# Performance work log

Hardware: AMD Instinct MI355X
Metric: run time of the kernel (lower is better)

The kernel has to match this reference:

```python
import jax, jax.numpy as jnp
import numpy as np

N_NODES = 100000
N_EDGES = 1600000
D = 128
LAYERS = 3
LN_EPS = 1e-5


def setup_inputs() -> dict:
    key = jax.random.key(0)
    k1, k2, k3 = jax.random.split(key, 3)
    x = jax.random.normal(k1, (N_NODES, D), dtype=jnp.float32)
    edge_index = jax.random.randint(k2, (2, N_EDGES), 0, N_NODES, dtype=jnp.int64)
    W = jax.random.normal(k3, (LAYERS, D, D), dtype=jnp.float32) * (1.0 / np.sqrt(D))
    b = jnp.zeros((LAYERS, D), dtype=jnp.float32)
    ln_w = jnp.ones((LAYERS, D), dtype=jnp.float32)
    ln_b = jnp.zeros((LAYERS, D), dtype=jnp.float32)
    return {"x": x, "edge_index": edge_index, "W": W, "b": b, "ln_w": ln_w, "ln_b": ln_b}


def _gcn_conv(x, row, col, deg_inv_sqrt, W, b):
    # x: [N, D]; row/col: [E+N] (self-loops appended); PyG GCNConv math:
    # h = (D^-1/2 (A+I) D^-1/2) (x @ W) + b
    xw = x @ W  # [N, D]
    norm = deg_inv_sqrt[row] * deg_inv_sqrt[col]  # [E+N]
    msg = xw[row] * norm[:, None]  # gather + scale, memory-bound
    out = jax.ops.segment_sum(msg, col, num_segments=x.shape[0])  # scatter-add at targets
    return out + b


def _layer_norm(h, w, bset):
    mu = jnp.mean(h, axis=-1, keepdims=True)
    var = jnp.mean(jnp.square(h - mu), axis=-1, keepdims=True)
    return (h - mu) * jax.lax.rsqrt(var + LN_EPS) * w + bset


def reference(x, edge_index, W, b, ln_w, ln_b):
    n = x.shape[0]
    loops = jnp.arange(n, dtype=edge_index.dtype)
    row = jnp.concatenate([edge_index[0], loops])  # sources
    col = jnpp = jnp.concatenate([edge_index[1], loops])  # targets
    deg = jax.ops.segment_sum(jnp.ones_like(col, dtype=x.dtype), col, num_segments=n)
    deg_inv_sqrt = jax.lax.rsqrt(deg)  # deg >= 1 due to self-loops
    for i in range(LAYERS):
        h = _gcn_conv(x, row, col, deg_inv_sqrt, W[i], b[i])
        h = jax.nn.relu(h)
        h = h + x  # residual (shapes always match: in == emb)
        # dropout is identity in eval mode
        x = _layer_norm(h, ln_w[i], ln_b[i])
    return x
```

## Files before the change

kernel.cpp:

```cpp
#include <hip/hip_runtime.h>
#include <stdint.h>

#define NN 100000
#define NE 1600000
#define DD 128
#define NLAYERS 3
#define NB 196
#define BRS 9
#define NBLK 256
#define EPB 6250
#define CAP 96
#define ENTCAP 9216
#define OVFCAP 4096
#define AGG_BLOCKS 2048

typedef __attribute__((ext_vector_type(8))) short bf16x8;
typedef __attribute__((ext_vector_type(4))) float f32x4;
typedef __attribute__((ext_vector_type(4))) unsigned int u32x4;
typedef __attribute__((ext_vector_type(2))) unsigned int u32x2;

__device__ __forceinline__ float bflo(uint32_t v){ return __uint_as_float(v << 16); }
__device__ __forceinline__ float bfhi(uint32_t v){ return __uint_as_float(v & 0xFFFF0000u); }
__device__ __forceinline__ float bf1(unsigned short u){ return __uint_as_float(((uint32_t)u) << 16); }
__device__ __forceinline__ unsigned short f2bf(float f){
  uint32_t u = __float_as_uint(f);
  u += 0x7FFFu + ((u >> 16) & 1u);
  return (unsigned short)(u >> 16);
}
__device__ __forceinline__ int colof(int j){ return ((j & 7) << 4) | (j >> 3); }

__global__ __launch_bounds__(256) void k_detect(const uint32_t* __restrict__ x,
                                                const uint32_t* __restrict__ ei,
                                                int* __restrict__ flags,
                                                int* __restrict__ ovf_cnt,
                                                unsigned int* __restrict__ gmax){
  __shared__ int s_f32, s_i32;
  if (threadIdx.x == 0){
    s_f32 = 0; s_i32 = 0; *ovf_cnt = 0;
    gmax[0] = 0u; gmax[1] = 0u; gmax[2] = 0u;
  }
  __syncthreads();
  int f = 0, i32 = 0;
  for (int idx = threadIdx.x; idx < 8192; idx += 256){
    uint32_t u = x[idx];
    if (((u >> 7) & 0xFFu) >= 0x90u) f++;
  }
  for (int idx = threadIdx.x; idx < 2048; idx += 256){
    if (ei[2*idx + 1] != 0u) i32++;
  }
  atomicAdd(&s_f32, f); atomicAdd(&s_i32, i32);
  __syncthreads();
  if (threadIdx.x == 0){
    flags[0] = (s_f32 > 100) ? 1 : 0;
    flags[1] = (s_i32 > 10) ? 0 : 1;
  }
}

__device__ __forceinline__ int load_edge(const int* ei, int i64m, size_t idx){
  if (i64m) return (int)((const uint32_t*)ei)[2*idx];
  return ei[idx];
}


__global__ __launch_bounds__(256) void k_params(const void* __restrict__ W, const void* __restrict__ b,
                                                const void* __restrict__ lnw, const void* __restrict__ lnb,
                                                const int* __restrict__ flags,
                                                unsigned short* __restrict__ wtP,
                                                float* __restrict__ pbP, float* __restrict__ plwP,
                                                float* __restrict__ plbP,
                                                uint8_t* __restrict__ yqc){
  int l = blockIdx.x;
  int f32m = flags[0];
  if (l == 0 && threadIdx.x < 32)
    ((uint32_t*)yqc)[(size_t)NN*32 + threadIdx.x] = 0x80808080u;
  for (int idx = threadIdx.x; idx < DD*DD; idx += 256){
    int c = idx >> 7, j = idx & 127;
    int src = colof(j)*DD + c;
    unsigned short v = f32m ? f2bf(((const float*)W)[l*DD*DD + src])
                            : ((const unsigned short*)W)[l*DD*DD + src];
    wtP[l*DD*DD + idx] = v;
  }
  for (int idx = threadIdx.x; idx < DD; idx += 256){
    int c = colof(idx);
    if (f32m){
      pbP [l*DD+idx] = ((const float*)b)[l*DD+c];
      plwP[l*DD+idx] = ((const float*)lnw)[l*DD+c];
      plbP[l*DD+idx] = ((const float*)lnb)[l*DD+c];
    } else {
      pbP [l*DD+idx] = bf1(((const unsigned short*)b)[l*DD+c]);
      plwP[l*DD+idx] = bf1(((const unsigned short*)lnw)[l*DD+c]);
      plbP[l*DD+idx] = bf1(((const unsigned short*)lnb)[l*DD+c]);
    }
  }
}

__global__ __launch_bounds__(256) void k_cvt(const void* __restrict__ x, const int* __restrict__ flags,
                                             unsigned short* __restrict__ xbP){
  size_t idx = (size_t)blockIdx.x*256 + threadIdx.x;
  size_t base = idx*8;
  if (base >= (size_t)NN*DD) return;
  int i = (int)(base >> 7), j0 = (int)(base & 127);
  unsigned short v[8];
  if (flags[0]){
    const float* xf = (const float*)x + (size_t)i*DD;
    #pragma unroll
    for (int t = 0; t < 8; ++t) v[t] = f2bf(xf[colof(j0+t)]);
  } else {
    const unsigned short* xs = (const unsigned short*)x + (size_t)i*DD;
    #pragma unroll
    for (int t = 0; t < 8; ++t) v[t] = xs[colof(j0+t)];
  }
  u32x4 o;
  o[0] = (uint32_t)v[0] | ((uint32_t)v[1] << 16);
  o[1] = (uint32_t)v[2] | ((uint32_t)v[3] << 16);
  o[2] = (uint32_t)v[4] | ((uint32_t)v[5] << 16);
  o[3] = (uint32_t)v[6] | ((uint32_t)v[7] << 16);
  *(u32x4*)(xbP + base) = o;
}

__global__ __launch_bounds__(256) void k_cells(const int* __restrict__ ei, const int* __restrict__ flags,
                                               uint32_t* __restrict__ cells, int* __restrict__ cellcnt,
                                               uint64_t* __restrict__ ovf, int* __restrict__ ovf_cnt){
  __shared__ int cnt[NB];
  int tid = threadIdx.x, blk = blockIdx.x;
  for (int b = tid; b < NB; b += 256) cnt[b] = 0;
  __syncthreads();
  int i64m = flags[1];
  int e0 = blk*EPB;
  for (int e = e0 + tid; e < e0 + EPB; e += 256){
    int c = load_edge(ei, i64m, (size_t)NE + e);
    if (c < 0) c = 0; if (c > NN-1) c = NN-1;
    int r = load_edge(ei, i64m, (size_t)e);
    if (r < 0) r = 0; if (r > NN-1) r = NN-1;
    int b = c >> BRS;
    uint32_t pack = ((uint32_t)r << BRS) | (uint32_t)(c & 511);
    int pos = atomicAdd(&cnt[b], 1);
    if (pos < CAP){
      cells[((size_t)blk*NB + b)*CAP + pos] = pack;
    } else {
      int op = atomicAdd(ovf_cnt, 1);
      if (op < OVFCAP) ovf[op] = ((uint64_t)b << 32) | (uint64_t)pack;
    }
  }
  __syncthreads();
  for (int b = tid; b < NB; b += 256){
    int v = cnt[b]; if (v > CAP) v = CAP;
    cellcnt[blk*NB + b] = v;
  }
}

__global__ __launch_bounds__(256) void k_btotal(const int* __restrict__ cellcnt,
                                                const uint64_t* __restrict__ ovf,
                                                const int* __restrict__ ovf_cnt,
                                                int* __restrict__ btot){
  int b = blockIdx.x, tid = threadIdx.x;
  int s = 0;
  for (int blk = tid; blk < NBLK; blk += 256) s += cellcnt[blk*NB + b];
  int oc = *ovf_cnt; if (oc > OVFCAP) oc = OVFCAP;
  for (int i = tid; i < oc; i += 256) if ((int)(ovf[i] >> 32) == b) s++;
  #pragma unroll
  for (int m = 1; m < 64; m <<= 1) s += __shfl_xor(s, m, 64);
  __shared__ int sm[4];
  int wid = tid >> 6, lane = tid & 63;
  if (lane == 0) sm[wid] = s;
  __syncthreads();
  if (tid == 0){
    int nvalid = NN - b*512; if (nvalid > 512) nvalid = 512; if (nvalid < 0) nvalid = 0;
    btot[b] = sm[0] + sm[1] + sm[2] + sm[3] + 8*nvalid;
  }
}

__global__ __launch_bounds__(256) void k_bscan(const int* __restrict__ btot,
                                               int* __restrict__ bbase, int* __restrict__ colptr){
  __shared__ int sm[256];
  int tid = threadIdx.x;
  int v = (tid < NB) ? btot[tid] : 0;
  sm[tid] = v; __syncthreads();
  for (int o = 1; o < 256; o <<= 1){
    int t = (tid >= o) ? sm[tid - o] : 0;
    __syncthreads();
    sm[tid] += t;
    __syncthreads();
  }
  if (tid < NB) bbase[tid] = sm[tid] - v;
  if (tid == 0){
    int tot = sm[NB-1];
    bbase[NB] = tot;
    colptr[NN] = tot;
  }
}

__global__ __launch_bounds__(256) void k_csr(const uint32_t* __restrict__ cells,
                                             const int* __restrict__ cellcnt,
                                             const uint64_t* __restrict__ ovf,
                                             const int* __restrict__ ovf_cnt,
                                             const int* __restrict__ bbase,
                                             int* __restrict__ csr, int* __restrict__ colptr,
                                             int* __restrict__ deg8, float* __restrict__ dis){
  __shared__ uint32_t ent[ENTCAP];
  __shared__ int cnt2[512];
  __shared__ int off[512];
  __shared__ int off0[512];
  __shared__ int m;
  int b = blockIdx.x, tid = threadIdx.x, lane = tid & 63, wid = tid >> 6;
  if (tid == 0) m = 0;
  for (int t = tid; t < 512; t += 256) cnt2[t] = 0;
  __syncthreads();
  {
    int blk = tid;
    int c = cellcnt[blk*NB + b];
    int base = atomicAdd(&m, c);
    const uint32_t* src = cells + ((size_t)blk*NB + b)*CAP;
    for (int k = 0; k < c; ++k){
      int p = base + k;
      if (p < ENTCAP) ent[p] = src[k];
    }
  }
  int oc = *ovf_cnt; if (oc > OVFCAP) oc = OVFCAP;
  for (int i = tid; i < oc; i += 256){
    uint64_t v = ovf[i];
    if ((int)(v >> 32) == b){
      int p = atomicAdd(&m, 1);
      if (p < ENTCAP) ent[p] = (uint32_t)v;
    }
  }
  __syncthreads();
  int mm = m; if (mm > ENTCAP) mm = ENTCAP;
  for (int i = tid; i < mm; i += 256) atomicAdd(&cnt2[ent[i] & 511], 1);
  __syncthreads();
  int nbase = b << BRS;
  if (wid == 0){
    int loc[8]; int s = 0;
    #pragma unroll
    for (int k = 0; k < 8; ++k){
      int idx = lane*8 + k;
      int padded = ((nbase + idx) < NN) ? ((cnt2[idx] + 8) & ~7) : 0;
      loc[k] = padded;
      s += padded;
    }
    int pref = s;
    #pragma unroll
    for (int d = 1; d < 64; d <<= 1){
      int t = __shfl_up(pref, d, 64);
      if (lane >= d) pref += t;
    }
    int run = pref - s;
    #pragma unroll
    for (int k = 0; k < 8; ++k){ off[lane*8 + k] = run; run += loc[k]; }
  }
  __syncthreads();
  int gb = bbase[b];
  for (int t = tid; t < 512; t += 256){
    int node = nbase + t;
    if (node < NN){
      int o = off[t];
      off0[t] = o;
      colptr[node] = gb + o;
      deg8[node] = (cnt2[t] + 8) & ~7;
      dis[node] = rsqrtf(1.0f + (float)cnt2[t]);
      csr[gb + o] = node;
      off[t] = o + 1;
    }
  }
  __syncthreads();
  for (int i = tid; i < mm; i += 256){
    uint32_t e = ent[i];
    int t = e & 511;
    int pos = atomicAdd(&off[t], 1);
    csr[gb + pos] = (int)(e >> BRS);
  }
  __syncthreads();
  for (int t = tid; t < 512; t += 256){
    int node = nbase + t;
    if (node < NN){
      int start = off0[t] + cnt2[t] + 1;
      int end   = off0[t] + ((cnt2[t] + 8) & ~7);
      for (int p2 = start; p2 < end; ++p2) csr[gb + p2] = NN;
    }
  }
}


__global__ __launch_bounds__(256) void k_gemm(const unsigned short* __restrict__ x,
                                              const unsigned short* __restrict__ wt,
                                              const float* __restrict__ dis,
                                              unsigned short* __restrict__ y,
                                              uint8_t* __restrict__ yqc,
                                              unsigned int* __restrict__ gmax, int layer){
  int wave = threadIdx.x >> 6, lane = threadIdx.x & 63;
  int lr = lane & 15, lk = lane >> 4;
  int r0 = blockIdx.x*64 + wave*16;
  int arow = r0 + lr; if (arow > NN-1) arow = NN-1;

  float inv = 0.f;
  if (layer > 0){
    float S = 1.25f * fmaxf(__uint_as_float(gmax[layer-1]), 1e-20f);
    inv = 127.0f / S;
  }

  f32x4 zero = {0.f, 0.f, 0.f, 0.f};
  f32x4 acc[8];
  #pragma unroll
  for (int cf = 0; cf < 8; ++cf) acc[cf] = zero;

  const bf16x8* xp = (const bf16x8*)(x + (size_t)arow*DD + lk*8);
  #pragma unroll
  for (int ks = 0; ks < 4; ++ks){
    bf16x8 a = xp[ks*4];
    #pragma unroll
    for (int cf = 0; cf < 8; ++cf){
      const bf16x8* wp = (const bf16x8*)(wt + (size_t)(cf*16 + lr)*DD + lk*8);
      bf16x8 bfr = wp[ks*4];
      acc[cf] = __builtin_amdgcn_mfma_f32_16x16x32_bf16(a, bfr, acc[cf], 0, 0, 0);
    }
  }

  float wmax = 0.f;
  #pragma unroll
  for (int t = 0; t < 4; ++t){
    int rr = r0 + lk*4 + t;
    int rc = rr > NN-1 ? NN-1 : rr;
    float ds = dis[rc];
    if (layer == 0){
      u32x4 pk;
      #pragma unroll
      for (int w = 0; w < 4; ++w){
        float v0 = acc[2*w][t]*ds, v1 = acc[2*w+1][t]*ds;
        wmax = fmaxf(wmax, fmaxf(fabsf(v0), fabsf(v1)));
        pk[w] = (uint32_t)f2bf(v0) | ((uint32_t)f2bf(v1) << 16);
      }
      if (rr < NN)
        *(u32x4*)(y + (size_t)rr*128 + lr*8) = pk;
    } else {
      uint32_t b0 = 0, b1 = 0;
      #pragma unroll
      for (int cf = 0; cf < 8; ++cf){
        float v = acc[cf][t]*ds;
        wmax = fmaxf(wmax, fabsf(v));
        int qv = (int)rintf(v*inv) + 128;
        qv = qv < 0 ? 0 : (qv > 255 ? 255 : qv);
        if (cf < 4) b0 |= (uint32_t)qv << (8*cf);
        else        b1 |= (uint32_t)qv << (8*(cf-4));
      }
      if (rr < NN){
        u32x2 pk; pk[0] = b0; pk[1] = b1;
        *(u32x2*)(yqc + (size_t)rr*128 + lr*8) = pk;
      }
    }
  }
  #pragma unroll
  for (int m = 1; m < 64; m <<= 1) wmax = fmaxf(wmax, __shfl_xor(wmax, m, 64));
  __shared__ float wm[4];
  if (lane == 0) wm[wave] = wmax;
  __syncthreads();
  if (threadIdx.x == 0){
    float bm = fmaxf(fmaxf(wm[0], wm[1]), fmaxf(wm[2], wm[3]));
    atomicMax(&gmax[layer], __float_as_uint(bm));
  }
}

__global__ __launch_bounds__(256) void k_quant(const unsigned short* __restrict__ y,
                                               uint8_t* __restrict__ yqc,
                                               const unsigned int* __restrict__ gmax, int layer){
  int idx = blockIdx.x*256 + threadIdx.x;
  if (idx >= NN*2) return;
  int r = idx >> 1, half = idx & 1;
  float gm = __uint_as_float(gmax[layer]);
  float sc = 127.0f / fmaxf(gm, 1e-20f);
  const unsigned short* row = y + (size_t)r*128 + half*64;
  uint8_t* dst = yqc + (size_t)r*128 + half*64;
  u32x4 in[8];
  #pragma unroll
  for (int c = 0; c < 8; ++c) in[c] = *(const u32x4*)(row + 8*c);
  u32x4 o[4];
  #pragma unroll
  for (int c = 0; c < 4; ++c){
    uint32_t qq[8];
    #pragma unroll
    for (int w = 0; w < 8; ++w){
      uint32_t d = in[c*2 + (w >> 2)][w & 3];
      int q0 = (int)rintf(bflo(d)*sc) + 128;
      int q1 = (int)rintf(bfhi(d)*sc) + 128;
      q0 = q0 < 0 ? 0 : (q0 > 255 ? 255 : q0);
      q1 = q1 < 0 ? 0 : (q1 > 255 ? 255 : q1);
      qq[w] = (uint32_t)q0 | ((uint32_t)q1 << 8);
    }
    o[c][0] = qq[0] | (qq[1] << 16);
    o[c][1] = qq[2] | (qq[3] << 16);
    o[c][2] = qq[4] | (qq[5] << 16);
    o[c][3] = qq[6] | (qq[7] << 16);
  }
  #pragma unroll
  for (int c = 0; c < 4; ++c)
    *(u32x4*)(dst + 16*c) = o[c];
}

__global__ __launch_bounds__(256) void k_agg(const uint8_t* __restrict__ yq,
                                             const unsigned int* __restrict__ gmax, int layer,
                                             unsigned short* __restrict__ xbP,
                                             void* __restrict__ out, int last,
                                             const int* __restrict__ flags,
                                             const int* __restrict__ colptr,
                                             const int* __restrict__ deg8,
                                             const int* __restrict__ csr,
                                             const float* __restrict__ dis,
                                             const float* __restrict__ bbP,
                                             const float* __restrict__ lnwP,
                                             const float* __restrict__ lnbP){
  __shared__ float sp[384];
  int tid = threadIdx.x;
  for (int idx = tid; idx < 384; idx += 256)
    sp[idx] = (idx < 128) ? bbP[idx] : (idx < 256) ? lnwP[idx-128] : lnbP[idx-256];
  __syncthreads();

  int lane = tid & 63;
  int k = lane >> 3, q = lane & 7;
  int sel0 = k & 1, sel1 = (k >> 1) & 1, sel2 = (k >> 2) & 1;
  int js = (sel0 << 2) | (sel1 << 1) | sel2;
  int w  = js & 3, dl = js >> 2;
  int d0 = 16*q + 4*w + dl;
  float G = ((layer == 0) ? __uint_as_float(gmax[0])
                          : 1.25f * __uint_as_float(gmax[layer-1])) * (1.0f/127.0f);
  int f32m = flags[0];

  for (int i = __builtin_amdgcn_readfirstlane(blockIdx.x*4 + (tid >> 6));
       i < NN; i += AGG_BLOCKS*4){
    int s2 = colptr[i];
    int n8 = deg8[i];
    float di = dis[i];

    uint32_t accA[4] = {0,0,0,0}, accB[4] = {0,0,0,0};
    int np = n8 >> 3;
    int p = 0;
    for (; p + 2 <= np; p += 2){
      int srcA = csr[s2 + p*8 + k];
      int srcB = csr[s2 + p*8 + 8 + k];
      u32x4 dvA = *(const u32x4*)(yq + (((uint32_t)srcA << 7) | (q << 4)));
      u32x4 dvB = *(const u32x4*)(yq + (((uint32_t)srcB << 7) | (q << 4)));
      #pragma unroll
      for (int ww = 0; ww < 4; ++ww){
        accA[ww] += dvA[ww] & 0x00FF00FFu;
        accB[ww] += (dvA[ww] >> 8) & 0x00FF00FFu;
        accA[ww] += dvB[ww] & 0x00FF00FFu;
        accB[ww] += (dvB[ww] >> 8) & 0x00FF00FFu;
      }
    }
    if (p < np){
      int src = csr[s2 + p*8 + k];
      u32x4 dv = *(const u32x4*)(yq + (((uint32_t)src << 7) | (q << 4)));
      #pragma unroll
      for (int ww = 0; ww < 4; ++ww){
        accA[ww] += dv[ww] & 0x00FF00FFu;
        accB[ww] += (dv[ww] >> 8) & 0x00FF00FFu;
      }
    }

    uint32_t K4[4];
    #pragma unroll
    for (int j = 0; j < 4; ++j){
      uint32_t g = sel0 ? accA[j] : accB[j];
      uint32_t r = __shfl_xor(g, 8, 64);
      K4[j] = (sel0 ? accB[j] : accA[j]) + r;
    }
    uint32_t K2[2];
    #pragma unroll
    for (int j = 0; j < 2; ++j){
      uint32_t g = sel1 ? K4[j] : K4[2+j];
      uint32_t r = __shfl_xor(g, 16, 64);
      K2[j] = (sel1 ? K4[2+j] : K4[j]) + r;
    }
    uint32_t g2 = sel2 ? K2[0] : K2[1];
    uint32_t r2 = __shfl_xor(g2, 32, 64);
    uint32_t fin = (sel2 ? K2[1] : K2[0]) + r2;

    float corr = 128.0f * (float)n8;
    float a0 = ((float)(fin & 0xFFFFu) - corr) * G;
    float a1 = ((float)(fin >> 16)     - corr) * G;

    float h0 = fmaxf(a0*di + sp[d0],     0.f) + bf1(xbP[(size_t)i*DD + d0]);
    float h1 = fmaxf(a1*di + sp[d0 + 2], 0.f) + bf1(xbP[(size_t)i*DD + d0 + 2]);

    float s1 = h0 + h1, s2v = h0*h0 + h1*h1;
    #pragma unroll
    for (int m = 1; m < 64; m <<= 1){
      s1  += __shfl_xor(s1, m, 64);
      s2v += __shfl_xor(s2v, m, 64);
    }
    float mean = s1*(1.f/128.f);
    float var  = s2v*(1.f/128.f) - mean*mean;
    float rstd = rsqrtf(var + 1e-5f);

    float o0 = (h0 - mean)*rstd*sp[128 + d0]     + sp[256 + d0];
    float o1 = (h1 - mean)*rstd*sp[128 + d0 + 2] + sp[256 + d0 + 2];

    if (!last){
      uint32_t mv = (uint32_t)f2bf(o0) | ((uint32_t)f2bf(o1) << 16);
      uint32_t pr = __shfl_xor(mv, 8, 64);
      if (dl == 0){
        u32x2 pk;
        pk[0] = (mv & 0xFFFFu) | (pr << 16);
        pk[1] = (mv >> 16) | (pr & 0xFFFF0000u);
        *(u32x2*)(xbP + (size_t)i*DD + d0) = pk;
      }
    } else {
      if (f32m){
        float* of = (float*)out + (size_t)i*DD;
        of[colof(d0)]     = o0;
        of[colof(d0 + 2)] = o1;
      } else {
        unsigned short* ob = (unsigned short*)out + (size_t)i*DD;
        ob[colof(d0)]     = f2bf(o0);
        ob[colof(d0 + 2)] = f2bf(o1);
      }
    }
  }
}


extern "C" void kernel_launch(void* const* d_in, const int* in_sizes, int n_in,
                              void* d_out, int out_size, void* d_ws, size_t ws_size,
                              hipStream_t stream){
  const void* x0  = d_in[0];
  const int*  ei  = (const int*)d_in[1];
  const void* W   = d_in[2];
  const void* b   = d_in[3];
  const void* lnw = d_in[4];
  const void* lnb = d_in[5];

  char* ws = (char*)d_ws;
  size_t off = 0;
  auto alloc = [&](size_t bytes)->char*{
    char* p = ws + off;
    off += (bytes + 255) & ~(size_t)255;
    return p;
  };
  unsigned short* xbP = (unsigned short*)alloc((size_t)NN*DD*2);
  char* regionA = ws + off;
  unsigned short* y = (unsigned short*)alloc((size_t)NN*256);
  unsigned short* wtP = (unsigned short*)alloc((size_t)NLAYERS*DD*DD*2);
  float* pbP  = (float*)alloc((size_t)NLAYERS*DD*4);
  float* plwP = (float*)alloc((size_t)NLAYERS*DD*4);
  float* plbP = (float*)alloc((size_t)NLAYERS*DD*4);
  size_t cellsBytes = (size_t)NBLK*NB*CAP*4;
  size_t usedA = (size_t)(ws + off - regionA);
  if (usedA < cellsBytes) off += cellsBytes - usedA;
  uint32_t* cells = (uint32_t*)regionA;
  uint8_t* yqc = (uint8_t*)alloc((size_t)(NN+1)*128);
  int* csr    = (int*)alloc((size_t)(NE + 8*NN)*4 + 256);
  int* colptr = (int*)alloc((size_t)(NN+1)*4);
  int* deg8   = (int*)alloc((size_t)NN*4);
  float* dis  = (float*)alloc((size_t)NN*4);
  int* cellcnt = (int*)alloc((size_t)NBLK*NB*4);
  int* btot    = (int*)alloc(NB*4);
  int* bbase   = (int*)alloc((NB+1)*4);
  uint64_t* ovf = (uint64_t*)alloc(OVFCAP*8);
  int* ovf_cnt  = (int*)alloc(256);
  int* flags = (int*)alloc(256);
  unsigned int* gmax = (unsigned int*)alloc(256);

  k_detect<<<1, 256, 0, stream>>>((const uint32_t*)x0, (const uint32_t*)ei, flags, ovf_cnt, gmax);
  k_cvt<<<(NN*DD/8 + 255)/256, 256, 0, stream>>>(x0, flags, xbP);
  k_cells<<<NBLK, 256, 0, stream>>>(ei, flags, cells, cellcnt, ovf, ovf_cnt);
  k_btotal<<<NB, 256, 0, stream>>>(cellcnt, ovf, ovf_cnt, btot);
  k_bscan<<<1, 256, 0, stream>>>(btot, bbase, colptr);
  k_csr<<<NB, 256, 0, stream>>>(cells, cellcnt, ovf, ovf_cnt, bbase, csr, colptr, deg8, dis);
  k_params<<<NLAYERS, 256, 0, stream>>>(W, b, lnw, lnb, flags, wtP, pbP, plwP, plbP, yqc);

  for (int l = 0; l < NLAYERS; ++l){
    k_gemm<<<(NN + 63)/64, 256, 0, stream>>>(xbP, wtP + (size_t)l*DD*DD, dis, y, yqc, gmax, l);
    if (l == 0)
      k_quant<<<(NN*2 + 255)/256, 256, 0, stream>>>(y, yqc, gmax, l);
    k_agg<<<AGG_BLOCKS, 256, 0, stream>>>(yqc, gmax, l, xbP, d_out,
                                    (l == NLAYERS-1) ? 1 : 0, flags, colptr, deg8, csr, dis,
                                    pbP + (size_t)l*DD, plwP + (size_t)l*DD, plbP + (size_t)l*DD);
  }
}
```

Baseline: 334.1 us.

## Fuse block total and scan kernels, split param prep, double GEMM rows per wave

Three separate changes. The block-total and prefix-scan kernels are merged into one single-block kernel in which each thread serially sums its bucket's cell counts, removing one launch. k_params is split across 8 blocks per layer to parallelise the weight transpose. k_gemm now has each wave compute two 16-row tiles that share each loaded weight fragment, halving weight loads per row and halving the grid, at the cost of more registers per thread.

```diff
diff --git a/kernel.cpp b/kernel.cpp
--- a/kernel.cpp
+++ b/kernel.cpp
@@ -69,27 +69,30 @@
                                                 float* __restrict__ pbP, float* __restrict__ plwP,
                                                 float* __restrict__ plbP,
                                                 uint8_t* __restrict__ yqc){
-  int l = blockIdx.x;
+  int l = blockIdx.x >> 3, part = blockIdx.x & 7;
   int f32m = flags[0];
-  if (l == 0 && threadIdx.x < 32)
+  if (blockIdx.x == 0 && threadIdx.x < 32)
     ((uint32_t*)yqc)[(size_t)NN*32 + threadIdx.x] = 0x80808080u;
-  for (int idx = threadIdx.x; idx < DD*DD; idx += 256){
+  int end = part*2048 + 2048;
+  for (int idx = part*2048 + threadIdx.x; idx < end; idx += 256){
     int c = idx >> 7, j = idx & 127;
     int src = colof(j)*DD + c;
     unsigned short v = f32m ? f2bf(((const float*)W)[l*DD*DD + src])
                             : ((const unsigned short*)W)[l*DD*DD + src];
     wtP[l*DD*DD + idx] = v;
   }
-  for (int idx = threadIdx.x; idx < DD; idx += 256){
-    int c = colof(idx);
-    if (f32m){
-      pbP [l*DD+idx] = ((const float*)b)[l*DD+c];
-      plwP[l*DD+idx] = ((const float*)lnw)[l*DD+c];
-      plbP[l*DD+idx] = ((const float*)lnb)[l*DD+c];
-    } else {
-      pbP [l*DD+idx] = bf1(((const unsigned short*)b)[l*DD+c]);
-      plwP[l*DD+idx] = bf1(((const unsigned short*)lnw)[l*DD+c]);
-      plbP[l*DD+idx] = bf1(((const unsigned short*)lnb)[l*DD+c]);
+  if (part == 0){
+    for (int idx = threadIdx.x; idx < DD; idx += 256){
+      int c = colof(idx);
+      if (f32m){
+        pbP [l*DD+idx] = ((const float*)b)[l*DD+c];
+        plwP[l*DD+idx] = ((const float*)lnw)[l*DD+c];
+        plbP[l*DD+idx] = ((const float*)lnb)[l*DD+c];
+      } else {
+        pbP [l*DD+idx] = bf1(((const unsigned short*)b)[l*DD+c]);
+        plwP[l*DD+idx] = bf1(((const unsigned short*)lnw)[l*DD+c]);
+        plbP[l*DD+idx] = bf1(((const unsigned short*)lnb)[l*DD+c]);
+      }
     }
   }
 }
@@ -149,32 +152,21 @@
   }
 }
 
-__global__ __launch_bounds__(256) void k_btotal(const int* __restrict__ cellcnt,
-                                                const uint64_t* __restrict__ ovf,
-                                                const int* __restrict__ ovf_cnt,
-                                                int* __restrict__ btot){
-  int b = blockIdx.x, tid = threadIdx.x;
-  int s = 0;
-  for (int blk = tid; blk < NBLK; blk += 256) s += cellcnt[blk*NB + b];
-  int oc = *ovf_cnt; if (oc > OVFCAP) oc = OVFCAP;
-  for (int i = tid; i < oc; i += 256) if ((int)(ovf[i] >> 32) == b) s++;
-  #pragma unroll
-  for (int m = 1; m < 64; m <<= 1) s += __shfl_xor(s, m, 64);
-  __shared__ int sm[4];
-  int wid = tid >> 6, lane = tid & 63;
-  if (lane == 0) sm[wid] = s;
-  __syncthreads();
-  if (tid == 0){
-    int nvalid = NN - b*512; if (nvalid > 512) nvalid = 512; if (nvalid < 0) nvalid = 0;
-    btot[b] = sm[0] + sm[1] + sm[2] + sm[3] + 8*nvalid;
-  }
-}
-
-__global__ __launch_bounds__(256) void k_bscan(const int* __restrict__ btot,
+__global__ __launch_bounds__(256) void k_scan1(const int* __restrict__ cellcnt,
+                                               const uint64_t* __restrict__ ovf,
+                                               const int* __restrict__ ovf_cnt,
                                                int* __restrict__ bbase, int* __restrict__ colptr){
   __shared__ int sm[256];
   int tid = threadIdx.x;
-  int v = (tid < NB) ? btot[tid] : 0;
+  int v = 0;
+  if (tid < NB){
+    int s = 0;
+    for (int blk = 0; blk < NBLK; ++blk) s += cellcnt[blk*NB + tid];
+    int oc = *ovf_cnt; if (oc > OVFCAP) oc = OVFCAP;
+    for (int i = 0; i < oc; ++i) if ((int)(ovf[i] >> 32) == tid) s++;
+    int nvalid = NN - tid*512; if (nvalid > 512) nvalid = 512; if (nvalid < 0) nvalid = 0;
+    v = s + 8*nvalid;
+  }
   sm[tid] = v; __syncthreads();
   for (int o = 1; o < 256; o <<= 1){
     int t = (tid >= o) ? sm[tid - o] : 0;
@@ -183,11 +175,7 @@
     __syncthreads();
   }
   if (tid < NB) bbase[tid] = sm[tid] - v;
-  if (tid == 0){
-    int tot = sm[NB-1];
-    bbase[NB] = tot;
-    colptr[NN] = tot;
-  }
+  if (tid == NB-1){ bbase[NB] = sm[tid]; colptr[NN] = sm[tid]; }
 }
 
 __global__ __launch_bounds__(256) void k_csr(const uint32_t* __restrict__ cells,
@@ -281,6 +269,41 @@
 }
 
 
+#define GEMM_EPI(ACC, RBASE)                                                        \
+  {                                                                                 \
+    _Pragma("unroll")                                                               \
+    for (int t = 0; t < 4; ++t){                                                    \
+      int rr = (RBASE) + lk*4 + t;                                                  \
+      int rc = rr > NN-1 ? NN-1 : rr;                                               \
+      float ds = dis[rc];                                                           \
+      if (layer == 0){                                                              \
+        u32x4 pk;                                                                   \
+        _Pragma("unroll")                                                           \
+        for (int w = 0; w < 4; ++w){                                                \
+          float v0 = ACC[2*w][t]*ds, v1 = ACC[2*w+1][t]*ds;                         \
+          wmax = fmaxf(wmax, fmaxf(fabsf(v0), fabsf(v1)));                          \
+          pk[w] = (uint32_t)f2bf(v0) | ((uint32_t)f2bf(v1) << 16);                  \
+        }                                                                           \
+        if (rr < NN) *(u32x4*)(y + (size_t)rr*128 + lr*8) = pk;                     \
+      } else {                                                                      \
+        uint32_t b0 = 0, b1 = 0;                                                    \
+        _Pragma("unroll")                                                           \
+        for (int cf = 0; cf < 8; ++cf){                                             \
+          float v = ACC[cf][t]*ds;                                                  \
+          wmax = fmaxf(wmax, fabsf(v));                                             \
+          int qv = (int)rintf(v*inv) + 128;                                         \
+          qv = qv < 0 ? 0 : (qv > 255 ? 255 : qv);                                  \
+          if (cf < 4) b0 |= (uint32_t)qv << (8*cf);                                 \
+          else        b1 |= (uint32_t)qv << (8*(cf-4));                             \
+        }                                                                           \
+        if (rr < NN){                                                               \
+          u32x2 pk; pk[0] = b0; pk[1] = b1;                                         \
+          *(u32x2*)(yqc + (size_t)rr*128 + lr*8) = pk;                              \
+        }                                                                           \
+      }                                                                             \
+    }                                                                               \
+  }
+
 __global__ __launch_bounds__(256) void k_gemm(const unsigned short* __restrict__ x,
                                               const unsigned short* __restrict__ wt,
                                               const float* __restrict__ dis,
@@ -289,8 +312,10 @@
                                               unsigned int* __restrict__ gmax, int layer){
   int wave = threadIdx.x >> 6, lane = threadIdx.x & 63;
   int lr = lane & 15, lk = lane >> 4;
-  int r0 = blockIdx.x*64 + wave*16;
-  int arow = r0 + lr; if (arow > NN-1) arow = NN-1;
+  int rA = blockIdx.x*128 + wave*16;
+  int rB = rA + 64;
+  int aA = rA + lr; if (aA > NN-1) aA = NN-1;
+  int aB = rB + lr; if (aB > NN-1) aB = NN-1;
 
   float inv = 0.f;
   if (layer > 0){
@@ -299,55 +324,29 @@
   }
 
   f32x4 zero = {0.f, 0.f, 0.f, 0.f};
-  f32x4 acc[8];
+  f32x4 accA[8], accB[8];
   #pragma unroll
-  for (int cf = 0; cf < 8; ++cf) acc[cf] = zero;
-
-  const bf16x8* xp = (const bf16x8*)(x + (size_t)arow*DD + lk*8);
+  for (int cf = 0; cf < 8; ++cf){ accA[cf] = zero; accB[cf] = zero; }
+
+  const bf16x8* xpA = (const bf16x8*)(x + (size_t)aA*DD + lk*8);
+  const bf16x8* xpB = (const bf16x8*)(x + (size_t)aB*DD + lk*8);
   #pragma unroll
   for (int ks = 0; ks < 4; ++ks){
-    bf16x8 a = xp[ks*4];
+    bf16x8 a0 = xpA[ks*4];
+    bf16x8 a1 = xpB[ks*4];
     #pragma unroll
     for (int cf = 0; cf < 8; ++cf){
       const bf16x8* wp = (const bf16x8*)(wt + (size_t)(cf*16 + lr)*DD + lk*8);
       bf16x8 bfr = wp[ks*4];
-      acc[cf] = __builtin_amdgcn_mfma_f32_16x16x32_bf16(a, bfr, acc[cf], 0, 0, 0);
+      accA[cf] = __builtin_amdgcn_mfma_f32_16x16x32_bf16(a0, bfr, accA[cf], 0, 0, 0);
+      accB[cf] = __builtin_amdgcn_mfma_f32_16x16x32_bf16(a1, bfr, accB[cf], 0, 0, 0);
     }
   }
 
   float wmax = 0.f;
-  #pragma unroll
-  for (int t = 0; t < 4; ++t){
-    int rr = r0 + lk*4 + t;
-    int rc = rr > NN-1 ? NN-1 : rr;
-    float ds = dis[rc];
-    if (layer == 0){
-      u32x4 pk;
-      #pragma unroll
-      for (int w = 0; w < 4; ++w){
-        float v0 = acc[2*w][t]*ds, v1 = acc[2*w+1][t]*ds;
-        wmax = fmaxf(wmax, fmaxf(fabsf(v0), fabsf(v1)));
-        pk[w] = (uint32_t)f2bf(v0) | ((uint32_t)f2bf(v1) << 16);
-      }
-      if (rr < NN)
-        *(u32x4*)(y + (size_t)rr*128 + lr*8) = pk;
-    } else {
-      uint32_t b0 = 0, b1 = 0;
-      #pragma unroll
-      for (int cf = 0; cf < 8; ++cf){
-        float v = acc[cf][t]*ds;
-        wmax = fmaxf(wmax, fabsf(v));
-        int qv = (int)rintf(v*inv) + 128;
-        qv = qv < 0 ? 0 : (qv > 255 ? 255 : qv);
-        if (cf < 4) b0 |= (uint32_t)qv << (8*cf);
-        else        b1 |= (uint32_t)qv << (8*(cf-4));
-      }
-      if (rr < NN){
-        u32x2 pk; pk[0] = b0; pk[1] = b1;
-        *(u32x2*)(yqc + (size_t)rr*128 + lr*8) = pk;
-      }
-    }
-  }
+  GEMM_EPI(accA, rA)
+  GEMM_EPI(accB, rB)
+
   #pragma unroll
   for (int m = 1; m < 64; m <<= 1) wmax = fmaxf(wmax, __shfl_xor(wmax, m, 64));
   __shared__ float wm[4];
@@ -551,7 +550,6 @@
   int* deg8   = (int*)alloc((size_t)NN*4);
   float* dis  = (float*)alloc((size_t)NN*4);
   int* cellcnt = (int*)alloc((size_t)NBLK*NB*4);
-  int* btot    = (int*)alloc(NB*4);
   int* bbase   = (int*)alloc((NB+1)*4);
   uint64_t* ovf = (uint64_t*)alloc(OVFCAP*8);
   int* ovf_cnt  = (int*)alloc(256);
@@ -561,13 +559,12 @@
   k_detect<<<1, 256, 0, stream>>>((const uint32_t*)x0, (const uint32_t*)ei, flags, ovf_cnt, gmax);
   k_cvt<<<(NN*DD/8 + 255)/256, 256, 0, stream>>>(x0, flags, xbP);
   k_cells<<<NBLK, 256, 0, stream>>>(ei, flags, cells, cellcnt, ovf, ovf_cnt);
-  k_btotal<<<NB, 256, 0, stream>>>(cellcnt, ovf, ovf_cnt, btot);
-  k_bscan<<<1, 256, 0, stream>>>(btot, bbase, colptr);
+  k_scan1<<<1, 256, 0, stream>>>(cellcnt, ovf, ovf_cnt, bbase, colptr);
   k_csr<<<NB, 256, 0, stream>>>(cells, cellcnt, ovf, ovf_cnt, bbase, csr, colptr, deg8, dis);
-  k_params<<<NLAYERS, 256, 0, stream>>>(W, b, lnw, lnb, flags, wtP, pbP, plwP, plbP, yqc);
+  k_params<<<NLAYERS*8, 256, 0, stream>>>(W, b, lnw, lnb, flags, wtP, pbP, plwP, plbP, yqc);
 
   for (int l = 0; l < NLAYERS; ++l){
-    k_gemm<<<(NN + 63)/64, 256, 0, stream>>>(xbP, wtP + (size_t)l*DD*DD, dis, y, yqc, gmax, l);
+    k_gemm<<<(NN + 127)/128, 256, 0, stream>>>(xbP, wtP + (size_t)l*DD*DD, dis, y, yqc, gmax, l);
     if (l == 0)
       k_quant<<<(NN*2 + 255)/256, 256, 0, stream>>>(y, yqc, gmax, l);
     k_agg<<<AGG_BLOCKS, 256, 0, stream>>>(yqc, gmax, l, xbP, d_out,
```

Result: faster. 314.6 us (-5.8%).
